# Kernel optimization log

Hardware: AMD Instinct MI355X
Metric: run time of the kernel (lower is better)

## Reference

```python
import jax, jax.numpy as jnp
import numpy as np

VOCAB, EMBED, SEQ, HID = 50000, 128, 200, 30
BATCH = 4096


def setup_inputs() -> dict:
    key = jax.random.key(0)
    ks = jax.random.split(key, 14)
    s = lambda fan_in: 1.0 / np.sqrt(fan_in)
    return {
        "tokens": jax.random.randint(ks[0], (BATCH, SEQ), 0, VOCAB, dtype=jnp.int32),
        "emb": jax.random.normal(ks[1], (VOCAB, EMBED), jnp.float32) * 0.05,
        "Wx": jax.random.normal(ks[2], (EMBED, HID), jnp.float32) * s(EMBED),
        "Wh": jax.random.normal(ks[3], (HID, HID), jnp.float32) * s(HID),
        "b_rnn": jnp.zeros((HID,), jnp.float32),
        "W1": jax.random.normal(ks[4], (HID, 128), jnp.float32) * s(HID),
        "b1": jnp.zeros((128,), jnp.float32),
        "W2": jax.random.normal(ks[5], (128, 64), jnp.float32) * s(128),
        "b2": jnp.zeros((64,), jnp.float32),
        "W3": jax.random.normal(ks[6], (64, 32), jnp.float32) * s(64),
        "b3": jnp.zeros((32,), jnp.float32),
        "Wo": jax.random.normal(ks[7], (32, 1), jnp.float32) * s(32),
        "bo": jnp.zeros((1,), jnp.float32),
    }


def reference(tokens, emb, Wx, Wh, b_rnn, W1, b1, W2, b2, W3, b3, Wo, bo):
    # Embedding lookup: [B, T, E]
    x = emb[tokens]
    # SimpleRNN (tanh), return last hidden state. Precompute input projection
    # once as a big GEMM, then scan the recurrence over time.
    xp = jnp.einsum("bte,eh->tbh", x, Wx) + b_rnn  # [T, B, H]
    h0 = jnp.zeros((tokens.shape[0], Wh.shape[0]), x.dtype)

    def step(h, xp_t):
        h_new = jnp.tanh(xp_t + h @ Wh)
        return h_new, None

    h_last, _ = jax.lax.scan(step, h0, xp)
    # Dense head (dropout layers are identity at inference).
    d1 = jax.nn.relu(h_last @ W1 + b1)
    d2 = jax.nn.relu(d1 @ W2 + b2)
    d3 = jax.nn.relu(d2 @ W3 + b3)
    return jax.nn.sigmoid(d3 @ Wo + bo)
```

## Files before the change

### kernel.cpp

```cpp
#include <hip/hip_runtime.h>
#include <math.h>

#define VOCAB 50000
#define EMBED 128
#define SEQ   200
#define HID   30
#define BATCH 4096

__device__ __forceinline__ float tanh_fast(float x) {
    float e = __expf(2.0f * x);
    return 1.0f - 2.0f / (e + 1.0f);
}

__global__ __launch_bounds__(256) void embproj_kernel(
    const float* __restrict__ emb, const float* __restrict__ Wx,
    const float* __restrict__ brnn, float* __restrict__ embP)
{
    __shared__ float WxL[EMBED * HID];
    __shared__ float bL[32];
    int tid = threadIdx.x;
    for (int i = tid; i < EMBED * HID; i += 256) WxL[i] = Wx[i];
    if (tid < HID) bL[tid] = brnn[tid];
    __syncthreads();

    int g  = tid >> 5;
    int j  = tid & 31;
    int jj = (j < HID) ? j : 0;
    int v0 = blockIdx.x * 32 + g * 4;

    int vr0 = min(v0 + 0, VOCAB - 1);
    int vr1 = min(v0 + 1, VOCAB - 1);
    int vr2 = min(v0 + 2, VOCAB - 1);
    int vr3 = min(v0 + 3, VOCAB - 1);
    const float4* e0 = (const float4*)(emb + (size_t)vr0 * EMBED);
    const float4* e1 = (const float4*)(emb + (size_t)vr1 * EMBED);
    const float4* e2 = (const float4*)(emb + (size_t)vr2 * EMBED);
    const float4* e3 = (const float4*)(emb + (size_t)vr3 * EMBED);

    float bj = (j < HID) ? bL[jj] : 0.0f;
    float acc[4][4];
    #pragma unroll
    for (int rr = 0; rr < 4; ++rr) {
        acc[rr][0] = bj; acc[rr][1] = 0.f; acc[rr][2] = 0.f; acc[rr][3] = 0.f;
    }

    #pragma unroll 4
    for (int q = 0; q < EMBED / 4; ++q) {
        float4 r0 = e0[q], r1 = e1[q], r2 = e2[q], r3 = e3[q];
        #pragma unroll
        for (int d = 0; d < 4; ++d) {
            float w = WxL[(4 * q + d) * HID + jj];
            acc[0][d] += (&r0.x)[d] * w;
            acc[1][d] += (&r1.x)[d] * w;
            acc[2][d] += (&r2.x)[d] * w;
            acc[3][d] += (&r3.x)[d] * w;
        }
    }
    if (j < HID) {
        #pragma unroll
        for (int rr = 0; rr < 4; ++rr) {
            if (v0 + rr < VOCAB)
                embP[(size_t)(v0 + rr) * HID + j] =
                    (acc[rr][0] + acc[rr][1]) + (acc[rr][2] + acc[rr][3]);
        }
    }
}

__global__ __launch_bounds__(256, 2) void rnn_head_kernel(
    const int* __restrict__ tokens, const float* __restrict__ embP,
    const float* __restrict__ Wh,
    const float* __restrict__ W1, const float* __restrict__ b1,
    const float* __restrict__ W2, const float* __restrict__ b2,
    const float* __restrict__ W3, const float* __restrict__ b3,
    const float* __restrict__ Wo, const float* __restrict__ bo,
    float* __restrict__ out)
{
    __shared__ int tokL[8][SEQ];
    __shared__ __align__(16) float hL[8][36];
    __shared__ float d1L[8][128];
    __shared__ float d2L[8][64];

    int tid  = threadIdx.x;
    int wv   = tid >> 6;
    int l    = tid & 63;
    int half = l >> 5;
    int j    = l & 31;
    int rloc = wv * 2 + half;
    int b    = blockIdx.x * 8 + rloc;

    for (int i = j; i < SEQ; i += 32)
        tokL[rloc][i] = tokens[(size_t)b * SEQ + i];

    hL[rloc][j] = 0.0f;

    float whc[HID];
    #pragma unroll
    for (int k = 0; k < HID; ++k) whc[k] = (j < HID) ? Wh[k * HID + j] : 0.0f;

    bool ld = (j < HID);
    float xq[8];
    #pragma unroll
    for (int s = 0; s < 8; ++s) {
        int tk = tokL[rloc][s];
        xq[s] = ld ? embP[(size_t)tk * HID + j] : 0.0f;
    }

    for (int t = 0; t < SEQ; t += 8) {
        #pragma unroll
        for (int s = 0; s < 8; ++s) {
            int tf = t + 8 + s; tf = (tf < SEQ) ? tf : SEQ - 1;
            int tkn = tokL[rloc][tf];

            float hv[32];
            const float4* h4 = (const float4*)(&hL[rloc][0]);
            #pragma unroll
            for (int qq = 0; qq < 8; ++qq) {
                float4 hh = h4[qq];
                hv[4*qq+0] = hh.x; hv[4*qq+1] = hh.y;
                hv[4*qq+2] = hh.z; hv[4*qq+3] = hh.w;
            }
            float a0 = xq[s], a1 = 0.0f;
            #pragma unroll
            for (int k = 0; k < HID; k += 2) {
                a0 += hv[k]     * whc[k];
                a1 += hv[k + 1] * whc[k + 1];
            }
            float hn = tanh_fast(a0 + a1);
            if (j < HID) hL[rloc][j] = hn;
            xq[s] = ld ? embP[(size_t)tkn * HID + j] : 0.0f;
        }
    }

    {
        #pragma unroll
        for (int qq = 0; qq < 4; ++qq) {
            int c = j + 32 * qq;
            float acc = b1[c];
            #pragma unroll
            for (int k = 0; k < HID; ++k) acc += hL[rloc][k] * W1[k * 128 + c];
            d1L[rloc][c] = fmaxf(acc, 0.0f);
        }
        #pragma unroll
        for (int qq = 0; qq < 2; ++qq) {
            int c = j + 32 * qq;
            float acc = b2[c];
            #pragma unroll 8
            for (int k = 0; k < 128; ++k) acc += d1L[rloc][k] * W2[k * 64 + c];
            d2L[rloc][c] = fmaxf(acc, 0.0f);
        }
        float acc3 = b3[j];
        #pragma unroll 8
        for (int k = 0; k < 64; ++k) acc3 += d2L[rloc][k] * W3[k * 32 + j];
        acc3 = fmaxf(acc3, 0.0f);
        float prod = acc3 * Wo[j];
        #pragma unroll
        for (int m = 16; m > 0; m >>= 1) prod += __shfl_xor(prod, m, 32);
        if (j == 0) out[b] = 1.0f / (1.0f + __expf(-(prod + bo[0])));
    }
}

extern "C" void kernel_launch(void* const* d_in, const int* in_sizes, int n_in,
                              void* d_out, int out_size, void* d_ws, size_t ws_size,
                              hipStream_t stream) {
    (void)in_sizes; (void)n_in; (void)out_size; (void)ws_size;
    const int*   tokens = (const int*)  d_in[0];
    const float* emb    = (const float*)d_in[1];
    const float* Wx     = (const float*)d_in[2];
    const float* Wh     = (const float*)d_in[3];
    const float* brnn   = (const float*)d_in[4];
    const float* W1     = (const float*)d_in[5];
    const float* b1     = (const float*)d_in[6];
    const float* W2     = (const float*)d_in[7];
    const float* b2     = (const float*)d_in[8];
    const float* W3     = (const float*)d_in[9];
    const float* b3     = (const float*)d_in[10];
    const float* Wo     = (const float*)d_in[11];
    const float* bo     = (const float*)d_in[12];
    float* out  = (float*)d_out;
    float* embP = (float*)d_ws;

    embproj_kernel<<<(VOCAB + 31) / 32, 256, 0, stream>>>(emb, Wx, brnn, embP);
    rnn_head_kernel<<<BATCH / 8, 256, 0, stream>>>(
        tokens, embP, Wh, W1, b1, W2, b2, W3, b3, Wo, bo, out);
}
```

Before: 116.4 us.

## Process two hidden units per lane with 16 lanes per sequence in RNN

The recurrence kernel now assigns 16 lanes per batch row, each computing two hidden units, so a 64-lane wave covers four rows and blocks shrink to 128 threads. This halves thread count per row and gives each lane more independent FMA work to hide latency, at the cost of doubled register use for Wh columns and inputs. The dense head is reorganised so 32-lane halves each process two rows sequentially. Compiler fences are added to keep shared-memory ordering within a wave, which relies on wave-synchronous execution.

```diff
diff --git a/kernel.cpp b/kernel.cpp
--- a/kernel.cpp
+++ b/kernel.cpp
@@ -6,6 +6,8 @@
 #define SEQ   200
 #define HID   30
 #define BATCH 4096
+
+#define COMPILER_FENCE() asm volatile("" ::: "memory")
 
 __device__ __forceinline__ float tanh_fast(float x) {
     float e = __expf(2.0f * x);
@@ -66,7 +68,7 @@
     }
 }
 
-__global__ __launch_bounds__(256, 2) void rnn_head_kernel(
+__global__ __launch_bounds__(128, 1) void rnn_head_kernel(
     const int* __restrict__ tokens, const float* __restrict__ embP,
     const float* __restrict__ Wh,
     const float* __restrict__ W1, const float* __restrict__ b1,
@@ -83,26 +85,33 @@
     int tid  = threadIdx.x;
     int wv   = tid >> 6;
     int l    = tid & 63;
-    int half = l >> 5;
-    int j    = l & 31;
-    int rloc = wv * 2 + half;
+    int q4   = l >> 4;
+    int jj   = l & 15;
+    int rloc = wv * 4 + q4;
+    int jB   = jj + 16;
     int b    = blockIdx.x * 8 + rloc;
 
-    for (int i = j; i < SEQ; i += 32)
+    for (int i = jj; i < SEQ; i += 16)
         tokL[rloc][i] = tokens[(size_t)b * SEQ + i];
 
-    hL[rloc][j] = 0.0f;
-
-    float whc[HID];
-    #pragma unroll
-    for (int k = 0; k < HID; ++k) whc[k] = (j < HID) ? Wh[k * HID + j] : 0.0f;
-
-    bool ld = (j < HID);
-    float xq[8];
+    hL[rloc][jj] = 0.0f;
+    hL[rloc][jB] = 0.0f;
+    COMPILER_FENCE();
+
+    float whcA[HID], whcB[HID];
+    #pragma unroll
+    for (int k = 0; k < HID; ++k) {
+        whcA[k] = Wh[k * HID + jj];
+        whcB[k] = (jB < HID) ? Wh[k * HID + jB] : 0.0f;
+    }
+
+    bool ldB = (jB < HID);
+    float xqA[8], xqB[8];
     #pragma unroll
     for (int s = 0; s < 8; ++s) {
         int tk = tokL[rloc][s];
-        xq[s] = ld ? embP[(size_t)tk * HID + j] : 0.0f;
+        xqA[s] = embP[(size_t)tk * HID + jj];
+        xqB[s] = ldB ? embP[(size_t)tk * HID + jB] : 0.0f;
     }
 
     for (int t = 0; t < SEQ; t += 8) {
@@ -112,50 +121,69 @@
             int tkn = tokL[rloc][tf];
 
             float hv[32];
-            const float4* h4 = (const float4*)(&hL[rloc][0]);
             #pragma unroll
             for (int qq = 0; qq < 8; ++qq) {
-                float4 hh = h4[qq];
+                float4 hh;
+                __builtin_memcpy(&hh, &hL[rloc][4 * qq], sizeof(float4));
                 hv[4*qq+0] = hh.x; hv[4*qq+1] = hh.y;
                 hv[4*qq+2] = hh.z; hv[4*qq+3] = hh.w;
             }
-            float a0 = xq[s], a1 = 0.0f;
+            float a0 = xqA[s], a1 = 0.0f;
+            float c0 = xqB[s], c1 = 0.0f;
             #pragma unroll
             for (int k = 0; k < HID; k += 2) {
-                a0 += hv[k]     * whc[k];
-                a1 += hv[k + 1] * whc[k + 1];
+                a0 += hv[k]     * whcA[k];
+                a1 += hv[k + 1] * whcA[k + 1];
+                c0 += hv[k]     * whcB[k];
+                c1 += hv[k + 1] * whcB[k + 1];
             }
-            float hn = tanh_fast(a0 + a1);
-            if (j < HID) hL[rloc][j] = hn;
-            xq[s] = ld ? embP[(size_t)tkn * HID + j] : 0.0f;
-        }
-    }
-
-    {
+            float hnA = tanh_fast(a0 + a1);
+            float hnB = tanh_fast(c0 + c1);
+            hL[rloc][jj] = hnA;
+            if (ldB) hL[rloc][jB] = hnB;
+            COMPILER_FENCE();
+
+            xqA[s] = embP[(size_t)tkn * HID + jj];
+            xqB[s] = ldB ? embP[(size_t)tkn * HID + jB] : 0.0f;
+        }
+    }
+
+    int half = l >> 5, l32 = l & 31;
+    #pragma unroll
+    for (int pp = 0; pp < 2; ++pp) {
+        int rh = wv * 4 + half * 2 + pp;
+        int bB = blockIdx.x * 8 + rh;
+        float hs[HID];
+        #pragma unroll
+        for (int k = 0; k < HID; ++k) hs[k] = hL[rh][k];
+
         #pragma unroll
         for (int qq = 0; qq < 4; ++qq) {
-            int c = j + 32 * qq;
+            int c = l32 + 32 * qq;
             float acc = b1[c];
             #pragma unroll
-            for (int k = 0; k < HID; ++k) acc += hL[rloc][k] * W1[k * 128 + c];
-            d1L[rloc][c] = fmaxf(acc, 0.0f);
-        }
+            for (int k = 0; k < HID; ++k) acc += hs[k] * W1[k * 128 + c];
+            d1L[rh][c] = fmaxf(acc, 0.0f);
+        }
+        COMPILER_FENCE();
         #pragma unroll
         for (int qq = 0; qq < 2; ++qq) {
-            int c = j + 32 * qq;
+            int c = l32 + 32 * qq;
             float acc = b2[c];
             #pragma unroll 8
-            for (int k = 0; k < 128; ++k) acc += d1L[rloc][k] * W2[k * 64 + c];
-            d2L[rloc][c] = fmaxf(acc, 0.0f);
-        }
-        float acc3 = b3[j];
+            for (int k = 0; k < 128; ++k) acc += d1L[rh][k] * W2[k * 64 + c];
+            d2L[rh][c] = fmaxf(acc, 0.0f);
+        }
+        COMPILER_FENCE();
+        float acc3 = b3[l32];
         #pragma unroll 8
-        for (int k = 0; k < 64; ++k) acc3 += d2L[rloc][k] * W3[k * 32 + j];
+        for (int k = 0; k < 64; ++k) acc3 += d2L[rh][k] * W3[k * 32 + l32];
         acc3 = fmaxf(acc3, 0.0f);
-        float prod = acc3 * Wo[j];
+        float prod = acc3 * Wo[l32];
         #pragma unroll
         for (int m = 16; m > 0; m >>= 1) prod += __shfl_xor(prod, m, 32);
-        if (j == 0) out[b] = 1.0f / (1.0f + __expf(-(prod + bo[0])));
+        if (l32 == 0) out[bB] = 1.0f / (1.0f + __expf(-(prod + bo[0])));
+        COMPILER_FENCE();
     }
 }
 
@@ -180,6 +208,6 @@
     float* embP = (float*)d_ws;
 
     embproj_kernel<<<(VOCAB + 31) / 32, 256, 0, stream>>>(emb, Wx, brnn, embP);
-    rnn_head_kernel<<<BATCH / 8, 256, 0, stream>>>(
+    rnn_head_kernel<<<BATCH / 8, 128, 0, stream>>>(
         tokens, embP, Wh, W1, b1, W2, b2, W3, b3, Wo, bo, out);
 }
```

Result: slower. 125.4 us (+7.8%).

## Keep RNN hidden state in registers using DPP rotations; restructure embedding projection

Applied to the files above, without the earlier changes.

The recurrent step now keeps each hidden element in a register. Each lane walks the hidden vector with DPP row-rotate and ds_swizzle cross-lane ops, using Wh columns pre-permuted to match the rotation order, so the per-step LDS write and read of the hidden state go away. The embedding projection is rewritten so that each thread owns one vocabulary row held in registers and reads a transposed Wx from global memory, which adds a small transpose kernel and a workspace region. The risks are high register pressure in the projection kernel (128 floats per thread), the correctness of the permutation across the 16-lane halves, and the extra kernel launch.

```diff
diff --git a/kernel.cpp b/kernel.cpp
--- a/kernel.cpp
+++ b/kernel.cpp
@@ -12,57 +12,55 @@
     return 1.0f - 2.0f / (e + 1.0f);
 }
 
+__device__ __forceinline__ int ror1_i(int x) {
+    return __builtin_amdgcn_update_dpp(0, x, 0x121, 0xF, 0xF, false);
+}
+__device__ __forceinline__ float ror1_f(float x) {
+    return __int_as_float(ror1_i(__float_as_int(x)));
+}
+__device__ __forceinline__ int swz16_i(int x) {
+    return __builtin_amdgcn_ds_swizzle(x, 0x401F);
+}
+__device__ __forceinline__ float swz16_f(float x) {
+    return __int_as_float(swz16_i(__float_as_int(x)));
+}
+
+__global__ __launch_bounds__(256) void wxT_kernel(
+    const float* __restrict__ Wx, float* __restrict__ WxT)
+{
+    int idx = blockIdx.x * 256 + threadIdx.x;
+    if (idx < EMBED * HID) {
+        int j = idx >> 7;
+        int e = idx & 127;
+        WxT[idx] = Wx[e * HID + j];
+    }
+}
+
 __global__ __launch_bounds__(256) void embproj_kernel(
-    const float* __restrict__ emb, const float* __restrict__ Wx,
+    const float* __restrict__ emb, const float* __restrict__ WxT,
     const float* __restrict__ brnn, float* __restrict__ embP)
 {
-    __shared__ float WxL[EMBED * HID];
-    __shared__ float bL[32];
-    int tid = threadIdx.x;
-    for (int i = tid; i < EMBED * HID; i += 256) WxL[i] = Wx[i];
-    if (tid < HID) bL[tid] = brnn[tid];
-    __syncthreads();
+    int v  = blockIdx.x * 256 + threadIdx.x;
+    int vc = min(v, VOCAB - 1);
+    const float4* e4 = (const float4*)(emb + (size_t)vc * EMBED);
 
-    int g  = tid >> 5;
-    int j  = tid & 31;
-    int jj = (j < HID) ? j : 0;
-    int v0 = blockIdx.x * 32 + g * 4;
+    float4 er[32];
+    #pragma unroll
+    for (int q = 0; q < 32; ++q) er[q] = e4[q];
 
-    int vr0 = min(v0 + 0, VOCAB - 1);
-    int vr1 = min(v0 + 1, VOCAB - 1);
-    int vr2 = min(v0 + 2, VOCAB - 1);
-    int vr3 = min(v0 + 3, VOCAB - 1);
-    const float4* e0 = (const float4*)(emb + (size_t)vr0 * EMBED);
-    const float4* e1 = (const float4*)(emb + (size_t)vr1 * EMBED);
-    const float4* e2 = (const float4*)(emb + (size_t)vr2 * EMBED);
-    const float4* e3 = (const float4*)(emb + (size_t)vr3 * EMBED);
-
-    float bj = (j < HID) ? bL[jj] : 0.0f;
-    float acc[4][4];
-    #pragma unroll
-    for (int rr = 0; rr < 4; ++rr) {
-        acc[rr][0] = bj; acc[rr][1] = 0.f; acc[rr][2] = 0.f; acc[rr][3] = 0.f;
-    }
-
-    #pragma unroll 4
-    for (int q = 0; q < EMBED / 4; ++q) {
-        float4 r0 = e0[q], r1 = e1[q], r2 = e2[q], r3 = e3[q];
+    #pragma unroll 2
+    for (int j = 0; j < HID; ++j) {
+        const float* wj = WxT + j * EMBED;
+        float a0 = brnn[j], a1 = 0.f, a2 = 0.f, a3 = 0.f;
         #pragma unroll
-        for (int d = 0; d < 4; ++d) {
-            float w = WxL[(4 * q + d) * HID + jj];
-            acc[0][d] += (&r0.x)[d] * w;
-            acc[1][d] += (&r1.x)[d] * w;
-            acc[2][d] += (&r2.x)[d] * w;
-            acc[3][d] += (&r3.x)[d] * w;
+        for (int q = 0; q < 32; ++q) {
+            a0 += er[q].x * wj[4 * q + 0];
+            a1 += er[q].y * wj[4 * q + 1];
+            a2 += er[q].z * wj[4 * q + 2];
+            a3 += er[q].w * wj[4 * q + 3];
         }
-    }
-    if (j < HID) {
-        #pragma unroll
-        for (int rr = 0; rr < 4; ++rr) {
-            if (v0 + rr < VOCAB)
-                embP[(size_t)(v0 + rr) * HID + j] =
-                    (acc[rr][0] + acc[rr][1]) + (acc[rr][2] + acc[rr][3]);
-        }
+        if (v < VOCAB)
+            embP[(size_t)v * HID + j] = (a0 + a1) + (a2 + a3);
     }
 }
 
@@ -75,8 +73,8 @@
     const float* __restrict__ Wo, const float* __restrict__ bo,
     float* __restrict__ out)
 {
-    __shared__ int tokL[8][SEQ];
-    __shared__ __align__(16) float hL[8][36];
+    __shared__ int   tokL[8][SEQ];
+    __shared__ float hL[8][32];
     __shared__ float d1L[8][128];
     __shared__ float d2L[8][64];
 
@@ -91,19 +89,28 @@
     for (int i = j; i < SEQ; i += 32)
         tokL[rloc][i] = tokens[(size_t)b * SEQ + i];
 
-    hL[rloc][j] = 0.0f;
+    bool colv = (j < HID);
 
-    float whc[HID];
-    #pragma unroll
-    for (int k = 0; k < HID; ++k) whc[k] = (j < HID) ? Wh[k * HID + j] : 0.0f;
+    float wA[16], wB[16];
+    {
+        int kA = j;
+        int kB = swz16_i(j);
+        #pragma unroll
+        for (int N = 0; N < 16; ++N) {
+            wA[N] = (colv && kA < HID) ? Wh[kA * HID + j] : 0.0f;
+            wB[N] = (colv && kB < HID) ? Wh[kB * HID + j] : 0.0f;
+            if (N < 15) { kA = ror1_i(kA); kB = ror1_i(kB); }
+        }
+    }
 
-    bool ld = (j < HID);
     float xq[8];
     #pragma unroll
     for (int s = 0; s < 8; ++s) {
         int tk = tokL[rloc][s];
-        xq[s] = ld ? embP[(size_t)tk * HID + j] : 0.0f;
+        xq[s] = colv ? embP[(size_t)tk * HID + j] : 0.0f;
     }
+
+    float hreg = 0.0f;
 
     for (int t = 0; t < SEQ; t += 8) {
         #pragma unroll
@@ -111,25 +118,23 @@
             int tf = t + 8 + s; tf = (tf < SEQ) ? tf : SEQ - 1;
             int tkn = tokL[rloc][tf];
 
-            float hv[32];
-            const float4* h4 = (const float4*)(&hL[rloc][0]);
+            float a0 = xq[s], a1 = 0.0f;
+            xq[s] = colv ? embP[(size_t)tkn * HID + j] : 0.0f;
+
+            float rA = hreg;
+            float rB = swz16_f(hreg);
             #pragma unroll
-            for (int qq = 0; qq < 8; ++qq) {
-                float4 hh = h4[qq];
-                hv[4*qq+0] = hh.x; hv[4*qq+1] = hh.y;
-                hv[4*qq+2] = hh.z; hv[4*qq+3] = hh.w;
-            }
-            float a0 = xq[s], a1 = 0.0f;
-            #pragma unroll
-            for (int k = 0; k < HID; k += 2) {
-                a0 += hv[k]     * whc[k];
-                a1 += hv[k + 1] * whc[k + 1];
+            for (int N = 0; N < 16; ++N) {
+                a0 += rA * wA[N];
+                a1 += rB * wB[N];
+                if (N < 15) { rA = ror1_f(rA); rB = ror1_f(rB); }
             }
             float hn = tanh_fast(a0 + a1);
-            if (j < HID) hL[rloc][j] = hn;
-            xq[s] = ld ? embP[(size_t)tkn * HID + j] : 0.0f;
+            hreg = colv ? hn : 0.0f;
         }
     }
+
+    hL[rloc][j] = hreg;
 
     {
         #pragma unroll
@@ -178,8 +183,10 @@
     const float* bo     = (const float*)d_in[12];
     float* out  = (float*)d_out;
     float* embP = (float*)d_ws;
+    float* WxT  = (float*)((char*)d_ws + 6000000);
 
-    embproj_kernel<<<(VOCAB + 31) / 32, 256, 0, stream>>>(emb, Wx, brnn, embP);
+    wxT_kernel<<<(EMBED * HID + 255) / 256, 256, 0, stream>>>(Wx, WxT);
+    embproj_kernel<<<(VOCAB + 255) / 256, 256, 0, stream>>>(emb, WxT, brnn, embP);
     rnn_head_kernel<<<BATCH / 8, 256, 0, stream>>>(
         tokens, embP, Wh, W1, b1, W2, b2, W3, b3, Wo, bo, out);
 }
```

After: 160.7 us. 1.38x slower.

## Prefetch tokens from global two stages ahead and widen recurrence dot-product ILP

Applied to the files above, without the earlier changes.

Drops the shared-memory token staging and instead keeps token ids in registers, loading them directly from global memory one 8-step block ahead of the embedding-projection gather. Each gather is issued before the recurrence math, with sched_barriers added to keep that ordering. The hidden dot product now uses four accumulators over 32 zero-padded weights, and tanh uses a fast divide. This shortens the dependent load chain and the serial FMA chain on the critical recurrence path, at the cost of more registers, redundant padded FMAs, and constrained compiler scheduling.

```diff
diff --git a/kernel.cpp b/kernel.cpp
--- a/kernel.cpp
+++ b/kernel.cpp
@@ -7,9 +7,11 @@
 #define HID   30
 #define BATCH 4096
 
+typedef float4 __attribute__((__may_alias__)) f4ma;
+
 __device__ __forceinline__ float tanh_fast(float x) {
     float e = __expf(2.0f * x);
-    return 1.0f - 2.0f / (e + 1.0f);
+    return 1.0f - __fdividef(2.0f, e + 1.0f);
 }
 
 __global__ __launch_bounds__(256) void embproj_kernel(
@@ -75,7 +77,6 @@
     const float* __restrict__ Wo, const float* __restrict__ bo,
     float* __restrict__ out)
 {
-    __shared__ int tokL[8][SEQ];
     __shared__ __align__(16) float hL[8][36];
     __shared__ float d1L[8][128];
     __shared__ float d2L[8][64];
@@ -88,46 +89,51 @@
     int rloc = wv * 2 + half;
     int b    = blockIdx.x * 8 + rloc;
 
-    for (int i = j; i < SEQ; i += 32)
-        tokL[rloc][i] = tokens[(size_t)b * SEQ + i];
+    const int* trow = tokens + (size_t)b * SEQ;
+    int jc = (j < HID) ? j : (HID - 1);
 
     hL[rloc][j] = 0.0f;
+    __builtin_amdgcn_sched_barrier(0);
 
-    float whc[HID];
+    float whc[32];
     #pragma unroll
-    for (int k = 0; k < HID; ++k) whc[k] = (j < HID) ? Wh[k * HID + j] : 0.0f;
+    for (int k = 0; k < 32; ++k)
+        whc[k] = (k < HID && j < HID) ? Wh[k * HID + j] : 0.0f;
 
-    bool ld = (j < HID);
     float xq[8];
+    int   tr[8];
     #pragma unroll
     for (int s = 0; s < 8; ++s) {
-        int tk = tokL[rloc][s];
-        xq[s] = ld ? embP[(size_t)tk * HID + j] : 0.0f;
+        xq[s] = embP[(size_t)trow[s] * HID + jc];
+        tr[s] = trow[8 + s];
     }
 
     for (int t = 0; t < SEQ; t += 8) {
         #pragma unroll
         for (int s = 0; s < 8; ++s) {
-            int tf = t + 8 + s; tf = (tf < SEQ) ? tf : SEQ - 1;
-            int tkn = tokL[rloc][tf];
-
             float hv[32];
-            const float4* h4 = (const float4*)(&hL[rloc][0]);
+            const f4ma* h4 = (const f4ma*)(&hL[rloc][0]);
             #pragma unroll
             for (int qq = 0; qq < 8; ++qq) {
-                float4 hh = h4[qq];
+                f4ma hh = h4[qq];
                 hv[4*qq+0] = hh.x; hv[4*qq+1] = hh.y;
                 hv[4*qq+2] = hh.z; hv[4*qq+3] = hh.w;
             }
-            float a0 = xq[s], a1 = 0.0f;
+            float a0 = xq[s], a1 = 0.0f, a2 = 0.0f, a3 = 0.0f;
+            xq[s] = embP[(size_t)tr[s] * HID + jc];
+            int tn = t + 16 + s; tn = (tn < SEQ) ? tn : SEQ - 1;
+            tr[s] = trow[tn];
+
             #pragma unroll
-            for (int k = 0; k < HID; k += 2) {
+            for (int k = 0; k < 32; k += 4) {
                 a0 += hv[k]     * whc[k];
                 a1 += hv[k + 1] * whc[k + 1];
+                a2 += hv[k + 2] * whc[k + 2];
+                a3 += hv[k + 3] * whc[k + 3];
             }
-            float hn = tanh_fast(a0 + a1);
+            float hn = tanh_fast((a0 + a1) + (a2 + a3));
             if (j < HID) hL[rloc][j] = hn;
-            xq[s] = ld ? embP[(size_t)tkn * HID + j] : 0.0f;
+            __builtin_amdgcn_sched_barrier(0);
         }
     }
 
```

After: 107.0 us. 1.09x faster.
